# Performance work log

Hardware: AMD Instinct MI355X
Metric: run time of the kernel (lower is better)

The kernel has to match this reference:

```python
import jax, jax.numpy as jnp
import numpy as np

J = 24  # fixed pooling window (SampleLength/N = 1200/50)


def setup_inputs() -> dict:
    key = jax.random.key(0)
    k1, k2, k3 = jax.random.split(key, 3)
    T, N, K, C = 786432, 50, 400, 10  # T = 32768 segments * J
    x = jax.random.normal(k1, (T, N), dtype=jnp.float32)
    W1 = jax.random.normal(k2, (K, N), dtype=jnp.float32) * 0.1
    W2 = jax.random.normal(k3, (C, K), dtype=jnp.float32) * 0.1
    return {"x": x, "W1": W1, "W2": W2}


def reference(x, W1, W2):
    # linear + relu: [T, N] @ [N, K] -> [T, K]
    local_features = jax.nn.relu(jnp.einsum('tn,kn->tk', x, W1))
    # fixed-window mean over consecutive J rows: [T, K] -> [T//J, K]
    T, K = local_features.shape
    features = local_features.reshape(T // J, J, K).mean(axis=1)
    # final linear: [T//J, K] @ [K, C] -> [T//J, C]
    logits = jnp.einsum('bk,ck->bc', features, W2)
    return logits
```

## Files before the change

kernel.cpp:

```cpp
#include <hip/hip_runtime.h>
#include <hip/hip_bf16.h>

#define T_TOTAL 786432
#define N_IN 50
#define K_FEAT 400
#define C_OUT 10
#define NSEG 32768

#define W1F_TASKS (25 * 2 * 64)
#define W2T_OFF_BYTES 51200
#define W2T_FLOATS (25 * 320)
#define W1F32_OFF_BYTES 98304
#define W1F32_TASKS (13 * 4 * 64)
#define W2P_OFF_BYTES 163840
#define W2P_TASKS (13 * 64)
#define PREP_TASKS (W1F_TASKS + W2T_FLOATS + W1F32_TASKS + W2P_TASKS)
#define WS_NEEDED (W2P_OFF_BYTES + (size_t)W2P_TASKS * 8 * 4)

typedef __bf16 bfx8 __attribute__((ext_vector_type(8)));
typedef short  s16x8 __attribute__((ext_vector_type(8)));
typedef float  f32x2 __attribute__((ext_vector_type(2)));
typedef float  f32x4 __attribute__((ext_vector_type(4)));
typedef float  f32x16 __attribute__((ext_vector_type(16)));

static __device__ __forceinline__ short f2bf(float f) {
    union { float f; unsigned u; } v; v.f = f;
    unsigned r = v.u + 0x7fffu + ((v.u >> 16) & 1u);
    return (short)(r >> 16);
}

__global__ void prep_kernel(const float* __restrict__ W1,
                            const float* __restrict__ W2,
                            short* __restrict__ w1f, float* __restrict__ w2t,
                            short* __restrict__ w1f32, float* __restrict__ w2p)
{
    const int gid = blockIdx.x * blockDim.x + threadIdx.x;
    if (gid < W1F_TASKS) {
        const int lane = gid & 63;
        const int s    = (gid >> 6) & 1;
        const int tile = gid >> 7;
        const int m16  = lane & 15;
        const int quad = lane >> 4;
        const float* row = W1 + (tile * 16 + m16) * N_IN;
        s16x8 v;
        #pragma unroll
        for (int j = 0; j < 8; ++j) {
            const int n = s * 32 + quad * 8 + j;
            v[j] = (n < N_IN) ? f2bf(row[n]) : (short)0;
        }
        *(s16x8*)&w1f[gid * 8] = v;
    } else if (gid < W1F_TASKS + W2T_FLOATS) {
        const int i   = gid - W1F_TASKS;
        const int j   = i / 320;
        const int tid = i - j * 320;
        const int o    = tid >> 4;
        const int part = tid & 15;
        const int seg  = (o >= 10) ? 1 : 0;
        const int cls  = o - seg * 10;
        w2t[i] = W2[cls * K_FEAT + part * 25 + j];
    } else if (gid < W1F_TASKS + W2T_FLOATS + W1F32_TASKS) {
        const int i    = gid - W1F_TASKS - W2T_FLOATS;
        const int lane = i & 63;
        const int fi   = i >> 6;
        const int ft   = fi >> 2;
        const int kt   = fi & 3;
        const int feat = ft * 32 + (lane & 31);
        const int cbase = kt * 16 + (lane >> 5) * 8;
        s16x8 v;
        #pragma unroll
        for (int j = 0; j < 8; ++j) {
            const int col = cbase + j;
            v[j] = (feat < K_FEAT && col < N_IN) ? f2bf(W1[feat * N_IN + col])
                                                 : (short)0;
        }
        *(s16x8*)&w1f32[i * 8] = v;
    } else if (gid < PREP_TASKS) {
        const int i    = gid - W1F_TASKS - W2T_FLOATS - W1F32_TASKS;
        const int lane = i & 63;
        const int ft   = i >> 6;
        const int m32  = lane & 31;
        const int h    = lane >> 5;
        const int feat = 32 * ft + m32;
        float v[8];
        #pragma unroll
        for (int c = 0; c < 8; ++c)
            v[c] = (c < 5 && feat < K_FEAT) ? W2[(h * 5 + c) * K_FEAT + feat]
                                            : 0.f;
        float4* dst = (float4*)&w2p[(size_t)i * 8];
        dst[0] = make_float4(v[0], v[1], v[2], v[3]);
        dst[1] = make_float4(v[4], v[5], v[6], v[7]);
    }
}

__global__ __launch_bounds__(256, 4) void phase1_kernel(
    const float* __restrict__ x, const short* __restrict__ w1f32,
    const float* __restrict__ w2p, float* __restrict__ out)
{
    __shared__ __align__(16) short xs[4 * 4800];
    const int tid  = threadIdx.x;
    const int lane = tid & 63;
    const int wv   = tid >> 6;
    const int m32  = lane & 31;
    const int h    = lane >> 5;
    const int chunk = blockIdx.x * 4 + wv;
    short* myxs = xs + wv * 4800;
    const s16x8* wf = (const s16x8*)w1f32;

    auto loadB = [&](s16x8* B, int ft) {
        #pragma unroll
        for (int kt = 0; kt < 4; ++kt) B[kt] = wf[(ft * 4 + kt) * 64 + lane];
    };

    s16x8 Bc[4];
    loadB(Bc, 0);

    {
        const float* xg = x + (size_t)chunk * 4800;
        #pragma unroll
        for (int i = 0; i < 19; ++i) {
            const int q = 64 * i + lane;
            if (i < 18 || lane < 48) {
                const float4 v = *(const float4*)(xg + 4 * q);
                int lo, hi;
                asm("v_cvt_pk_bf16_f32 %0, %1, %2" : "=v"(lo) : "v"(v.x), "v"(v.y));
                asm("v_cvt_pk_bf16_f32 %0, %1, %2" : "=v"(hi) : "v"(v.z), "v"(v.w));
                int2 pk; pk.x = lo; pk.y = hi;
                *(int2*)&myxs[4 * q] = pk;
            }
        }
    }
    asm volatile("s_waitcnt lgkmcnt(0)" ::: "memory");
    __builtin_amdgcn_sched_barrier(0);

    s16x8 Af[3][4];
    #pragma unroll
    for (int rt = 0; rt < 3; ++rt) {
        const int row = 32 * rt + m32;
        const short* rp = myxs + row * 50 + 8 * h;
        #pragma unroll
        for (int kt = 0; kt < 3; ++kt) {
            int d0 = *(const int*)(rp + 16 * kt + 0);
            int d1 = *(const int*)(rp + 16 * kt + 2);
            int d2 = *(const int*)(rp + 16 * kt + 4);
            int d3 = *(const int*)(rp + 16 * kt + 6);
            int4 di = {d0, d1, d2, d3};
            Af[rt][kt] = __builtin_bit_cast(s16x8, di);
        }
        int dt = 0;
        if (h == 0) dt = *(const int*)(myxs + row * 50 + 48);
        int4 di3 = {dt, 0, 0, 0};
        Af[rt][3] = __builtin_bit_cast(s16x8, di3);
    }

    const int segbase = chunk * 4;

    f32x2 oaccp[2][5];
    #pragma unroll
    for (int g = 0; g < 2; ++g)
        #pragma unroll
        for (int k = 0; k < 5; ++k) { oaccp[g][k][0] = 0.f; oaccp[g][k][1] = 0.f; }

    const f32x2 z2 = {0.f, 0.f};

    for (int ft = 0; ft < 13; ++ft) {
        const float* wl = w2p + (size_t)(ft * 64 + lane) * 8;
        const float4 wa = *(const float4*)wl;
        const float  w4 = wl[4];

        float s0 = 0.f, s1 = 0.f, s2 = 0.f, s3 = 0.f;
        #pragma unroll
        for (int rt = 0; rt < 3; ++rt) {
            f32x16 acc;
            #pragma unroll
            for (int r = 0; r < 16; ++r) acc[r] = 0.f;
            __builtin_amdgcn_s_setprio(1);
            #pragma unroll
            for (int kt = 0; kt < 4; ++kt)
                acc = __builtin_amdgcn_mfma_f32_32x32x16_bf16(
                        __builtin_bit_cast(bfx8, Af[rt][kt]),
                        __builtin_bit_cast(bfx8, Bc[kt]), acc, 0, 0, 0);
            __builtin_amdgcn_s_setprio(0);
            f32x2 cv0 = z2, cv1 = z2;
            #pragma unroll
            for (int p = 0; p < 8; ++p) {
                f32x2 v2; v2[0] = acc[2 * p]; v2[1] = acc[2 * p + 1];
                v2 = __builtin_elementwise_max(v2, z2);
                if ((p >> 1) < 3 - rt) cv0 += v2; else cv1 += v2;
            }
            const float c0 = cv0[0] + cv0[1];
            const float c1 = cv1[0] + cv1[1];
            if (rt == 0)      { s0 += c0; s1 += c1; }
            else if (rt == 1) { s1 += c0; s2 += c1; }
            else              { s2 += c0; s3 += c1; }
        }
        if (ft < 12) loadB(Bc, ft + 1);

        s0 += __shfl_xor(s0, 32);
        s1 += __shfl_xor(s1, 32);
        s2 += __shfl_xor(s2, 32);
        s3 += __shfl_xor(s3, 32);

        const float wc[5] = {wa.x, wa.y, wa.z, wa.w, w4};
        const f32x2 q01 = {s0, s1};
        const f32x2 q23 = {s2, s3};
        #pragma unroll
        for (int k = 0; k < 5; ++k) {
            const f32x2 wk = {wc[k], wc[k]};
            oaccp[0][k] = __builtin_elementwise_fma(q01, wk, oaccp[0][k]);
            oaccp[1][k] = __builtin_elementwise_fma(q23, wk, oaccp[1][k]);
        }
    }

    float red[2][5][2];
    #pragma unroll
    for (int g = 0; g < 2; ++g)
        #pragma unroll
        for (int k = 0; k < 5; ++k)
            #pragma unroll
            for (int p = 0; p < 2; ++p) {
                float v = oaccp[g][k][p];
                v += __shfl_xor(v, 1);
                v += __shfl_xor(v, 2);
                v += __shfl_xor(v, 4);
                v += __shfl_xor(v, 8);
                v += __shfl_xor(v, 16);
                red[g][k][p] = v;
            }
    if (m32 == 0) {
        #pragma unroll
        for (int g = 0; g < 2; ++g)
            #pragma unroll
            for (int k = 0; k < 5; ++k)
                #pragma unroll
                for (int p = 0; p < 2; ++p)
                    out[(size_t)(segbase + 2 * g + p) * C_OUT + h * 5 + k] =
                        red[g][k][p] * (1.0f / 24.0f);
    }
}

#define FB_CPB 4
#define FB_NTHREADS 320
#define FB_XS_STRIDE 72
#define FB_XS_ROWS (FB_CPB * 48)

__global__ __launch_bounds__(FB_NTHREADS) void classifier_fb(
    const float* __restrict__ x, const short* __restrict__ w1f,
    const float* __restrict__ w2t, float* __restrict__ out)
{
    __shared__ short xs[FB_XS_ROWS * FB_XS_STRIDE];
    __shared__ float pooled[2 * K_FEAT];

    const int tid  = threadIdx.x;
    const int wave = tid >> 6;
    const int lane = tid & 63;
    const int m16  = lane & 15;
    const int quad = lane >> 4;

    {
        const float* xb = x + (size_t)blockIdx.x * (FB_XS_ROWS * N_IN);
        #pragma unroll
        for (int it = 0; it < (FB_XS_ROWS * 25) / FB_NTHREADS; ++it) {
            const int i = tid + it * FB_NTHREADS;
            const int r = i / 25;
            const int c2 = i - r * 25;
            const float2 v = *(const float2*)(xb + 2 * i);
            const int packed = (unsigned short)f2bf(v.x) |
                               ((unsigned)(unsigned short)f2bf(v.y) << 16);
            *(int*)&xs[r * FB_XS_STRIDE + 2 * c2] = packed;
        }
        for (int i = tid; i < FB_XS_ROWS * 7; i += FB_NTHREADS) {
            const int r = i / 7;
            const int c = 50 + 2 * (i - r * 7);
            *(int*)&xs[r * FB_XS_STRIDE + c] = 0;
        }
    }

    s16x8 bfrag[5][2];
    {
        const s16x8* wf = (const s16x8*)w1f;
        #pragma unroll
        for (int t = 0; t < 5; ++t)
            #pragma unroll
            for (int s = 0; s < 2; ++s)
                bfrag[t][s] = wf[((wave * 5 + t) * 2 + s) * 64 + lane];
    }

    const int o    = tid >> 4;
    const int part = tid & 15;
    const int segO = (o >= 10) ? 1 : 0;
    const int cls  = o - segO * 10;
    float w2r[25];
    #pragma unroll
    for (int j = 0; j < 25; ++j) w2r[j] = w2t[j * FB_NTHREADS + tid];

    __syncthreads();

    for (int ciq = 0; ciq < FB_CPB; ++ciq) {
        s16x8 a[3][2];
        #pragma unroll
        for (int r = 0; r < 3; ++r) {
            const short* arow =
                &xs[(ciq * 48 + r * 16 + m16) * FB_XS_STRIDE + quad * 8];
            a[r][0] = *(const s16x8*)(arow);
            a[r][1] = *(const s16x8*)(arow + 32);
        }
        #pragma unroll
        for (int t = 0; t < 5; ++t) {
            float c0 = 0.f, c1 = 0.f;
            #pragma unroll
            for (int r = 0; r < 3; ++r) {
                f32x4 acc = {0.f, 0.f, 0.f, 0.f};
                acc = __builtin_amdgcn_mfma_f32_16x16x32_bf16(
                        __builtin_bit_cast(bfx8, a[r][0]),
                        __builtin_bit_cast(bfx8, bfrag[t][0]), acc, 0, 0, 0);
                acc = __builtin_amdgcn_mfma_f32_16x16x32_bf16(
                        __builtin_bit_cast(bfx8, a[r][1]),
                        __builtin_bit_cast(bfx8, bfrag[t][1]), acc, 0, 0, 0);
                const float s = fmaxf(acc[0], 0.f) + fmaxf(acc[1], 0.f)
                              + fmaxf(acc[2], 0.f) + fmaxf(acc[3], 0.f);
                if (r * 4 + quad < 6) c0 += s; else c1 += s;
            }
            c0 += __shfl_xor(c0, 16); c0 += __shfl_xor(c0, 32);
            c1 += __shfl_xor(c1, 16); c1 += __shfl_xor(c1, 32);
            if (quad == 0) {
                const int feat = (wave * 5 + t) * 16 + m16;
                pooled[feat] = c0;
                pooled[K_FEAT + feat] = c1;
            }
        }
        __syncthreads();

        float sum = 0.f;
        const float* pv = &pooled[segO * K_FEAT + part * 25];
        #pragma unroll
        for (int j = 0; j < 25; ++j) sum += pv[j] * w2r[j];
        sum += __shfl_down(sum, 8, 16);
        sum += __shfl_down(sum, 4, 16);
        sum += __shfl_down(sum, 2, 16);
        sum += __shfl_down(sum, 1, 16);
        if (part == 0) {
            const int chunk = blockIdx.x * FB_CPB + ciq;
            out[(chunk * 2 + segO) * C_OUT + cls] = sum * (1.0f / 24.0f);
        }
        __syncthreads();
    }
}

extern "C" void kernel_launch(void* const* d_in, const int* in_sizes, int n_in,
                              void* d_out, int out_size, void* d_ws, size_t ws_size,
                              hipStream_t stream) {
    const float* x  = (const float*)d_in[0];
    const float* W1 = (const float*)d_in[1];
    const float* W2 = (const float*)d_in[2];
    float* out = (float*)d_out;

    short* w1f   = (short*)d_ws;
    float* w2t   = (float*)((char*)d_ws + W2T_OFF_BYTES);
    short* w1f32 = (short*)((char*)d_ws + W1F32_OFF_BYTES);
    float* w2p   = (float*)((char*)d_ws + W2P_OFF_BYTES);

    prep_kernel<<<(PREP_TASKS + 255) / 256, 256, 0, stream>>>(W1, W2, w1f, w2t,
                                                              w1f32, w2p);

    if (ws_size >= WS_NEEDED) {
        phase1_kernel<<<2048, 256, 0, stream>>>(x, w1f32, w2p, out);
    } else {
        classifier_fb<<<4096, FB_NTHREADS, 0, stream>>>(x, w1f, w2t, out);
    }
}
```

Baseline: 255.6 us.

## Drop per-tile half-wave shuffles by applying all ten W2 classes per lane

Each lane now holds all 10 W2 weights for its feature, so the cross-half shuffles of the per-segment sums inside the feature-tile loop go away. Instead, 4x5 packed FMA accumulators collect partial logits and are reduced once at the end, with an extra xor-32 shuffle step. The W2 packing layout changes to 12 floats per feature. This uses more registers, so launch bounds drop to 3 waves per SIMD, and the final reduction does 40 shuffle chains instead of 20.

```diff
diff --git a/kernel.cpp b/kernel.cpp
--- a/kernel.cpp
+++ b/kernel.cpp
@@ -13,9 +13,9 @@
 #define W1F32_OFF_BYTES 98304
 #define W1F32_TASKS (13 * 4 * 64)
 #define W2P_OFF_BYTES 163840
-#define W2P_TASKS (13 * 64)
+#define W2P_TASKS (13 * 32)
 #define PREP_TASKS (W1F_TASKS + W2T_FLOATS + W1F32_TASKS + W2P_TASKS)
-#define WS_NEEDED (W2P_OFF_BYTES + (size_t)W2P_TASKS * 8 * 4)
+#define WS_NEEDED (W2P_OFF_BYTES + (size_t)W2P_TASKS * 12 * 4)
 
 typedef __bf16 bfx8 __attribute__((ext_vector_type(8)));
 typedef short  s16x8 __attribute__((ext_vector_type(8)));
@@ -76,23 +76,21 @@
         *(s16x8*)&w1f32[i * 8] = v;
     } else if (gid < PREP_TASKS) {
         const int i    = gid - W1F_TASKS - W2T_FLOATS - W1F32_TASKS;
-        const int lane = i & 63;
-        const int ft   = i >> 6;
-        const int m32  = lane & 31;
-        const int h    = lane >> 5;
+        const int ft   = i >> 5;
+        const int m32  = i & 31;
         const int feat = 32 * ft + m32;
-        float v[8];
-        #pragma unroll
-        for (int c = 0; c < 8; ++c)
-            v[c] = (c < 5 && feat < K_FEAT) ? W2[(h * 5 + c) * K_FEAT + feat]
-                                            : 0.f;
-        float4* dst = (float4*)&w2p[(size_t)i * 8];
+        float v[12];
+        #pragma unroll
+        for (int c = 0; c < 12; ++c)
+            v[c] = (c < C_OUT && feat < K_FEAT) ? W2[c * K_FEAT + feat] : 0.f;
+        float4* dst = (float4*)&w2p[(size_t)i * 12];
         dst[0] = make_float4(v[0], v[1], v[2], v[3]);
         dst[1] = make_float4(v[4], v[5], v[6], v[7]);
-    }
-}
-
-__global__ __launch_bounds__(256, 4) void phase1_kernel(
+        dst[2] = make_float4(v[8], v[9], v[10], v[11]);
+    }
+}
+
+__global__ __launch_bounds__(256, 3) void phase1_kernel(
     const float* __restrict__ x, const short* __restrict__ w1f32,
     const float* __restrict__ w2p, float* __restrict__ out)
 {
@@ -154,18 +152,19 @@
 
     const int segbase = chunk * 4;
 
-    f32x2 oaccp[2][5];
+    f32x2 oacc[4][5];
     #pragma unroll
-    for (int g = 0; g < 2; ++g)
-        #pragma unroll
-        for (int k = 0; k < 5; ++k) { oaccp[g][k][0] = 0.f; oaccp[g][k][1] = 0.f; }
+    for (int s = 0; s < 4; ++s)
+        #pragma unroll
+        for (int k = 0; k < 5; ++k) { oacc[s][k][0] = 0.f; oacc[s][k][1] = 0.f; }
 
     const f32x2 z2 = {0.f, 0.f};
 
     for (int ft = 0; ft < 13; ++ft) {
-        const float* wl = w2p + (size_t)(ft * 64 + lane) * 8;
+        const float* wl = w2p + (size_t)(ft * 32 + m32) * 12;
         const float4 wa = *(const float4*)wl;
-        const float  w4 = wl[4];
+        const float4 wb = *(const float4*)(wl + 4);
+        const float2 wc2 = *(const float2*)(wl + 8);
 
         float s0 = 0.f, s1 = 0.f, s2 = 0.f, s3 = 0.f;
         #pragma unroll
@@ -195,46 +194,46 @@
         }
         if (ft < 12) loadB(Bc, ft + 1);
 
-        s0 += __shfl_xor(s0, 32);
-        s1 += __shfl_xor(s1, 32);
-        s2 += __shfl_xor(s2, 32);
-        s3 += __shfl_xor(s3, 32);
-
-        const float wc[5] = {wa.x, wa.y, wa.z, wa.w, w4};
-        const f32x2 q01 = {s0, s1};
-        const f32x2 q23 = {s2, s3};
+        f32x2 wp[5];
+        wp[0][0] = wa.x; wp[0][1] = wa.y;
+        wp[1][0] = wa.z; wp[1][1] = wa.w;
+        wp[2][0] = wb.x; wp[2][1] = wb.y;
+        wp[3][0] = wb.z; wp[3][1] = wb.w;
+        wp[4][0] = wc2.x; wp[4][1] = wc2.y;
+        const f32x2 sv0 = {s0, s0}, sv1 = {s1, s1}, sv2 = {s2, s2}, sv3 = {s3, s3};
         #pragma unroll
         for (int k = 0; k < 5; ++k) {
-            const f32x2 wk = {wc[k], wc[k]};
-            oaccp[0][k] = __builtin_elementwise_fma(q01, wk, oaccp[0][k]);
-            oaccp[1][k] = __builtin_elementwise_fma(q23, wk, oaccp[1][k]);
-        }
-    }
-
-    float red[2][5][2];
+            oacc[0][k] = __builtin_elementwise_fma(sv0, wp[k], oacc[0][k]);
+            oacc[1][k] = __builtin_elementwise_fma(sv1, wp[k], oacc[1][k]);
+            oacc[2][k] = __builtin_elementwise_fma(sv2, wp[k], oacc[2][k]);
+            oacc[3][k] = __builtin_elementwise_fma(sv3, wp[k], oacc[3][k]);
+        }
+    }
+
     #pragma unroll
-    for (int g = 0; g < 2; ++g)
+    for (int s = 0; s < 4; ++s)
         #pragma unroll
         for (int k = 0; k < 5; ++k)
             #pragma unroll
             for (int p = 0; p < 2; ++p) {
-                float v = oaccp[g][k][p];
+                float v = oacc[s][k][p];
                 v += __shfl_xor(v, 1);
                 v += __shfl_xor(v, 2);
                 v += __shfl_xor(v, 4);
                 v += __shfl_xor(v, 8);
                 v += __shfl_xor(v, 16);
-                red[g][k][p] = v;
-            }
-    if (m32 == 0) {
-        #pragma unroll
-        for (int g = 0; g < 2; ++g)
+                v += __shfl_xor(v, 32);
+                oacc[s][k][p] = v;
+            }
+    if (lane == 0) {
+        #pragma unroll
+        for (int s = 0; s < 4; ++s)
             #pragma unroll
             for (int k = 0; k < 5; ++k)
                 #pragma unroll
                 for (int p = 0; p < 2; ++p)
-                    out[(size_t)(segbase + 2 * g + p) * C_OUT + h * 5 + k] =
-                        red[g][k][p] * (1.0f / 24.0f);
+                    out[(size_t)(segbase + s) * C_OUT + 2 * k + p] =
+                        oacc[s][k][p] * (1.0f / 24.0f);
     }
 }
 
```

After: 255.1 us. Within noise of the previous version (-0.2%).
